# Kernel optimization log

Measured on AMD Instinct MI355X. Metric: run time of the kernel, lower is better.

Reference implementation:

```python
import jax, jax.numpy as jnp
import numpy as np

NEG = -1e9
ALPHA = 0.2  # LeakyReLU slope


def layer_norm(x, scale, bias, eps=1e-5):
    mu = jnp.mean(x, axis=-1, keepdims=True)
    var = jnp.mean(jnp.square(x - mu), axis=-1, keepdims=True)
    return (x - mu) * jax.lax.rsqrt(var + eps) * scale + bias


def gat_layer(x, adj, W, a):
    # x: (b, n, f_in); W: (h, f_in, d_k); a: (h, 2*d_k, 1); adj: (b, n, n) int
    d_k = W.shape[-1]
    h = jnp.einsum('bni,hio->bhno', x, W)            # (b, h, n, d_k)
    a_src = a[:, :d_k, 0]                            # (h, d_k)
    a_dst = a[:, d_k:, 0]                            # (h, d_k)
    # e[b,h,i,j] = leakyrelu(a_src.h_i + a_dst.h_j) -- split form of a.[h_i||h_j]
    src = jnp.einsum('bhnd,hd->bhn', h, a_src)
    dst = jnp.einsum('bhnd,hd->bhn', h, a_dst)
    e = jax.nn.leaky_relu(src[:, :, :, None] + dst[:, :, None, :], ALPHA)
    e = jnp.where(adj[:, None, :, :] == 0, NEG, e)   # mask non-edges
    att = jax.nn.softmax(e, axis=-1)                 # (b, h, n, n)
    return jnp.einsum('bhnm,bhmd->bhnd', att, h)     # (b, h, n, d_k)


def setup_inputs() -> dict:
    key = jax.random.key(0)
    ks = jax.random.split(key, 8)
    B, N, F_IN, HID, OUT, H = 4, 2048, 128, 256, 256, 4
    dk1 = HID // H
    dk2 = OUT // H
    xavier = lambda k, shp: jax.random.uniform(
        k, shp, jnp.float32, -1.0, 1.0) * np.sqrt(6.0 / (shp[-2] + shp[-1]))
    return {
        'node_features': jax.random.normal(ks[0], (B, N, F_IN), jnp.float32),
        'adjacency_matrix': jax.random.randint(ks[1], (B, N, N), 0, 2, jnp.int32),
        'Wp': jax.random.normal(ks[2], (F_IN, HID), jnp.float32) / np.sqrt(F_IN),
        'bp': jnp.zeros((HID,), jnp.float32),
        'W1': xavier(ks[3], (H, HID, dk1)),
        'a1': xavier(ks[4], (H, 2 * dk1, 1)),
        'ln1_s': jnp.ones((HID,), jnp.float32),
        'ln1_b': jnp.zeros((HID,), jnp.float32),
        'W2': xavier(ks[5], (H, HID, dk2)),
        'a2': xavier(ks[6], (H, 2 * dk2, 1)),
        'ln2_s': jnp.ones((dk2,), jnp.float32),
        'ln2_b': jnp.zeros((dk2,), jnp.float32),
    }


def reference(node_features, adjacency_matrix, Wp, bp, W1, a1, ln1_s, ln1_b,
              W2, a2, ln2_s, ln2_b):
    # input projection (dropout is identity in eval mode)
    x = node_features @ Wp + bp                       # (b, n, hid)
    b, n, _ = x.shape

    # layer 1: concat heads, LN, ELU, residual
    hp = gat_layer(x, adjacency_matrix, W1, a1)       # (b, h, n, dk1)
    x1 = hp.reshape(b, n, -1)                         # memory-order reshape (matches torch .view)
    x1 = layer_norm(x1, ln1_s, ln1_b)
    x1 = jax.nn.elu(x1)
    x = x + x1                                        # same shape -> residual

    # layer 2: mean over heads, LN
    hp = gat_layer(x, adjacency_matrix, W2, a2)       # (b, h, n, dk2)
    x2 = hp.mean(axis=1)                              # (b, n, dk2)
    x2 = layer_norm(x2, ln2_s, ln2_b)
    return x2
```

## Files before the change

kernel.cpp:

```cpp
#include <hip/hip_runtime.h>
#include <hip/hip_bf16.h>
#include <hip/hip_fp16.h>

#define BB   4
#define NN   2048
#define FIN  128
#define HD   256
#define NH   4
#define DK   64
#define NEGV (-1000000000.0f)
#define LOG2E 1.4426950408889634f

typedef _Float16 f16x8 __attribute__((ext_vector_type(8)));
typedef _Float16 f16x4 __attribute__((ext_vector_type(4)));
typedef __fp16   h16x2 __attribute__((ext_vector_type(2)));
typedef __fp16   h16x4 __attribute__((ext_vector_type(4)));
typedef __fp16   h16x8 __attribute__((ext_vector_type(8)));
typedef float    f32x16 __attribute__((ext_vector_type(16)));
typedef unsigned long long u64;

__device__ __forceinline__ int SWZ9(int b){ return b ^ (((b >> 9) & 7) << 4); }
__device__ __forceinline__ int SWZ8(int b){ return b ^ (((b >> 8) & 7) << 4); }

__device__ __forceinline__ float fexp2(float x){
#if __has_builtin(__builtin_amdgcn_exp2f)
  return __builtin_amdgcn_exp2f(x);
#else
  return __exp2f(x);
#endif
}

__device__ __forceinline__ f16x8 pack8(float4 a, float4 b){
  f16x8 r;
  r[0]=(_Float16)a.x; r[1]=(_Float16)a.y; r[2]=(_Float16)a.z; r[3]=(_Float16)a.w;
  r[4]=(_Float16)b.x; r[5]=(_Float16)b.y; r[6]=(_Float16)b.z; r[7]=(_Float16)b.w;
  return r;
}

__global__ void __launch_bounds__(256) k_setup(const int* __restrict__ adj,
                                               const float* __restrict__ Wp,
                                               const float* __restrict__ W1,
                                               const float* __restrict__ a1,
                                               const float* __restrict__ W2,
                                               const float* __restrict__ a2,
                                               u64* __restrict__ maskT,
                                               _Float16* __restrict__ WTF,
                                               _Float16* __restrict__ WpF,
                                               float* __restrict__ aS){
  int bid = blockIdx.x;
  int t = threadIdx.x;
  if (bid < 2048){
    int w = t >> 6, lane = t & 63;
    int row = bid*4 + w;
    int b = row >> 11, n = row & (NN-1);
    const int4* ar = (const int4*)(adj + (size_t)row*NN);
    int g = lane >> 4, q = lane & 15;
    #pragma unroll 2
    for (int step = 0; step < 8; ++step){
      int4 v = ar[step*64 + lane];
      unsigned nib = (unsigned)((v.x!=0) | ((v.y!=0)<<1) | ((v.z!=0)<<2) | ((v.w!=0)<<3));
      unsigned lo = (q < 8) ? (nib << (q*4)) : 0u;
      unsigned hi = (q < 8) ? 0u : (nib << ((q-8)*4));
      #pragma unroll
      for (int off = 1; off < 16; off <<= 1){
        lo |= __shfl_xor(lo, off);
        hi |= __shfl_xor(hi, off);
      }
      if (q == 0) maskT[(size_t)(b*32 + step*4 + g)*NN + n] = ((u64)hi << 32) | lo;
    }
  } else if (bid < 2056){
    int qq = bid - 2048;
    int lay = qq >> 2, hh = qq & 3;
    const float* W = (lay ? W2 : W1) + (size_t)hh*HD*DK;
    const float* a = (lay ? a2 : a1) + (size_t)hh*2*DK;
    _Float16* wf = WTF + (size_t)qq*32*512;
    int j = t*2;
    int l5 = j >> 4, lh = (j >> 3) & 1, e = j & 7;
    #pragma unroll 4
    for (int f = 0; f < 32; ++f){
      int kk = f >> 1, dh = f & 1;
      wf[f*512 + j]     = (_Float16)W[(kk*16 + lh*8 + e    )*DK + dh*32 + l5];
      wf[f*512 + j + 1] = (_Float16)W[(kk*16 + lh*8 + e + 1)*DK + dh*32 + l5];
    }
    if (t < 128) aS[(size_t)qq*128 + t] = a[t] * LOG2E;
  } else {
    int kk = bid - 2056;
    int j = t*2;
    int l5 = j >> 4, lh = (j >> 3) & 1, e = j & 7;
    #pragma unroll 4
    for (int cs = 0; cs < 8; ++cs){
      WpF[(kk*8 + cs)*512 + j]     = (_Float16)Wp[(kk*16 + lh*8 + e    )*HD + cs*32 + l5];
      WpF[(kk*8 + cs)*512 + j + 1] = (_Float16)Wp[(kk*16 + lh*8 + e + 1)*HD + cs*32 + l5];
    }
  }
}

template<int L1>
__global__ void __launch_bounds__(256) k_head4(const float* __restrict__ xin,
                                               const _Float16* __restrict__ WpF,
                                               const _Float16* __restrict__ WTF,
                                               const float* __restrict__ aS,
                                               const float* __restrict__ bp,
                                               float* __restrict__ xout,
                                               _Float16* __restrict__ hT,
                                               float* __restrict__ src,
                                               float* __restrict__ dst){
  int nt = blockIdx.x & 31;
  int bh = blockIdx.x >> 5;
  int b = bh >> 2, hh = bh & 3;
  int n0 = nt * 64;
  int t = threadIdx.x;
  int w = t >> 6, l = t & 63, lh = l >> 5, l5 = l & 31;
  int wr = w >> 1, wc = w & 1;

  __shared__ __align__(16) char sm[50176];

  if (L1){
    {
      int r = t >> 2, c0 = (t & 3) * 32;
      const float* np = xin + ((size_t)(b*NN) + n0 + r)*FIN + c0;
      #pragma unroll
      for (int u = 0; u < 4; ++u){
        float4 v0 = *(const float4*)&np[u*8];
        float4 v1 = *(const float4*)&np[u*8 + 4];
        *(f16x8*)&sm[32768 + SWZ8(r*256 + (c0 + u*8)*2)] = pack8(v0, v1);
      }
    }
    __syncthreads();
    f32x16 p00 = {}, p01 = {}, p10 = {}, p11 = {};
    #pragma unroll
    for (int kk = 0; kk < 8; ++kk){
      int ab = (kk*16 + lh*8)*2;
      f16x8 A0 = *(const f16x8*)&sm[32768 + SWZ8(l5*256 + ab)];
      f16x8 A1 = *(const f16x8*)&sm[32768 + SWZ8((32 + l5)*256 + ab)];
      const char* bf = (const char*)WpF + (size_t)(kk*8 + w*2)*1024 + l5*32 + lh*16;
      f16x8 B0 = *(const f16x8*)bf;
      f16x8 B1 = *(const f16x8*)(bf + 1024);
      p00 = __builtin_amdgcn_mfma_f32_32x32x16_f16(A0, B0, p00, 0, 0, 0);
      p01 = __builtin_amdgcn_mfma_f32_32x32x16_f16(A0, B1, p01, 0, 0, 0);
      p10 = __builtin_amdgcn_mfma_f32_32x32x16_f16(A1, B0, p10, 0, 0, 0);
      p11 = __builtin_amdgcn_mfma_f32_32x32x16_f16(A1, B1, p11, 0, 0, 0);
    }
    int c0a = w*64 + l5;
    float bp0 = bp[c0a], bp1 = bp[c0a + 32];
    size_t ro = ((size_t)(b*NN) + n0)*HD;
    #pragma unroll
    for (int g = 0; g < 16; ++g){
      int rr = (g & 3) + 8*(g >> 2) + 4*lh;
      float v00 = p00[g] + bp0, v01 = p01[g] + bp1;
      float v10 = p10[g] + bp0, v11 = p11[g] + bp1;
      *(_Float16*)&sm[SWZ9(rr*512 + c0a*2)]             = (_Float16)v00;
      *(_Float16*)&sm[SWZ9(rr*512 + (c0a + 32)*2)]      = (_Float16)v01;
      *(_Float16*)&sm[SWZ9((rr+32)*512 + c0a*2)]        = (_Float16)v10;
      *(_Float16*)&sm[SWZ9((rr+32)*512 + (c0a + 32)*2)] = (_Float16)v11;
      if (hh == 0){
        xout[ro + (size_t)rr*HD + c0a]           = v00;
        xout[ro + (size_t)rr*HD + c0a + 32]      = v01;
        xout[ro + (size_t)(rr+32)*HD + c0a]      = v10;
        xout[ro + (size_t)(rr+32)*HD + c0a + 32] = v11;
      }
    }
    __syncthreads();
  } else {
    int r = t >> 2, ks = (t & 3) * 64;
    const float* xp = &xin[((size_t)(b*NN) + n0 + r)*HD + ks];
    #pragma unroll
    for (int u = 0; u < 8; ++u){
      float4 v0 = *(const float4*)&xp[u*8];
      float4 v1 = *(const float4*)&xp[u*8 + 4];
      *(f16x8*)&sm[SWZ9(r*512 + (ks + u*8)*2)] = pack8(v0, v1);
    }
    __syncthreads();
  }

  f32x16 hA = {}, hB = {};
  const char* wtb = (const char*)WTF + (size_t)hh*32768 + wc*1024 + l5*32 + lh*16;
  #pragma unroll
  for (int kk = 0; kk < 16; kk += 2){
    int ab0 = (kk*16 + lh*8)*2;
    int ab1 = ((kk+1)*16 + lh*8)*2;
    f16x8 A0 = *(const f16x8*)&sm[SWZ9((wr*32 + l5)*512 + ab0)];
    f16x8 A1 = *(const f16x8*)&sm[SWZ9((wr*32 + l5)*512 + ab1)];
    f16x8 B0 = *(const f16x8*)(wtb + (size_t)kk*2048);
    f16x8 B1 = *(const f16x8*)(wtb + (size_t)(kk+1)*2048);
    hA = __builtin_amdgcn_mfma_f32_32x32x16_f16(A0, B0, hA, 0, 0, 0);
    hB = __builtin_amdgcn_mfma_f32_32x32x16_f16(A1, B1, hB, 0, 0, 0);
  }
  f32x16 acc = hA + hB;

  __syncthreads();
  _Float16* ls = (_Float16*)sm;
  int col = wc*32 + l5;
  float as = aS[(size_t)hh*128 + col];
  float ad = aS[(size_t)hh*128 + 64 + col];
  float* sd = (float*)(sm + 49152);
  #pragma unroll
  for (int g = 0; g < 16; ++g){
    int row = wr*32 + (g & 3) + 8*(g >> 2) + 4*lh;
    ls[col*80 + row] = (_Float16)acc[g];
    float sv = acc[g] * as;
    float dv = acc[g] * ad;
    #pragma unroll
    for (int o = 16; o >= 1; o >>= 1){ sv += __shfl_xor(sv, o); dv += __shfl_xor(dv, o); }
    if (l5 == 0){
      sd[wc*64 + row]       = sv;
      sd[128 + wc*64 + row] = dv;
    }
  }
  __syncthreads();
  int dd = t >> 2, part = t & 3;
  f16x8 o0 = *(const f16x8*)&ls[dd*80 + part*16];
  f16x8 o1 = *(const f16x8*)&ls[dd*80 + part*16 + 8];
  int base = part*1024 + (dd >> 5)*512 + (dd & 31)*16;
  _Float16* op = hT + (size_t)bh*131072 + (size_t)nt*4096 + base;
  *(f16x8*)op = o0;
  *(f16x8*)(op + 8) = o1;
  if (t < 64){
    src[bh*NN + n0 + t] = sd[t] + sd[64 + t];
    dst[bh*NN + n0 + t] = sd[128 + t] + sd[192 + t];
  }
}

__global__ void __launch_bounds__(256, 4) k_attn8(const float* __restrict__ src,
                                                  const float* __restrict__ dst,
                                                  const _Float16* __restrict__ hT,
                                                  const u64* __restrict__ maskT,
                                                  _Float16* __restrict__ accB,
                                                  float* __restrict__ psB){
  int ms = blockIdx.x & 1;
  int rb = (blockIdx.x >> 1) & 63;
  int bh = blockIdx.x >> 7;
  int b  = bh >> 2;
  int n0 = rb * 32;
  int t = threadIdx.x;
  int w = t >> 6, l = t & 63;
  int lh = l >> 5, l5 = l & 31;

  __shared__ __align__(16) char smem[9728];
  __shared__ float rs[4][32];
  __shared__ float red[4];
  float* dstS = (float*)smem;
  float* cs   = (float*)smem;

  {
    const float* dp = dst + bh*NN;
    float4 a = *(const float4*)&dp[t*4];
    float4 bq = *(const float4*)&dp[1024 + t*4];
    float mloc = fmaxf(fmaxf(fmaxf(a.x,a.y), fmaxf(a.z,a.w)),
                       fmaxf(fmaxf(bq.x,bq.y), fmaxf(bq.z,bq.w)));
    *(float4*)&dstS[t*4] = ms ? bq : a;
    #pragma unroll
    for (int o = 32; o >= 1; o >>= 1) mloc = fmaxf(mloc, __shfl_xor(mloc, o));
    if (l == 0) red[w] = mloc;
  }
  __syncthreads();
  float Mbh = fmaxf(fmaxf(red[0], red[1]), fmaxf(red[2], red[3]));
  float srcv = src[bh*NN + n0 + l5];
  float bv = srcv + Mbh;
  float bnd = fmaxf(bv, 0.2f*bv);
  float2 ps2 = make_float2(0.f, 0.f);
  f32x16 acc0 = {}, acc1 = {};

  int kb = w*16 + lh*8;
  const u64* mp = maskT + (size_t)(b*32 + ms*16)*NN + n0 + l5;
  const char* gB0 = (const char*)hT + (size_t)bh*262144 + ms*131072
                    + w*2048 + l5*32 + lh*16;

  u64 mkS0 = mp[0];
  f16x8 B0S0 = *(const f16x8*)(gB0);
  f16x8 B1S0 = *(const f16x8*)(gB0 + 1024);
  u64 mkS1 = mp[NN];
  f16x8 B0S1 = *(const f16x8*)(gB0 + 8192);
  f16x8 B1S1 = *(const f16x8*)(gB0 + 8192 + 1024);
  __builtin_amdgcn_sched_barrier(0);

  #pragma unroll
  for (int mt = 0; mt < 16; ++mt){
    u64 mkC = mkS0;
    f16x8 B0C = B0S0, B1C = B1S0;
    mkS0 = mkS1; B0S0 = B0S1; B1S0 = B1S1;
    if (mt < 14){
      mkS1 = mp[(size_t)(mt+2)*NN];
      B0S1 = *(const f16x8*)(gB0 + (size_t)(mt+2)*8192);
      B1S1 = *(const f16x8*)(gB0 + (size_t)(mt+2)*8192 + 1024);
    }
    __builtin_amdgcn_sched_barrier(0);
    float4 dq0 = *(const float4*)&dstS[mt*64 + kb];
    float4 dq1 = *(const float4*)&dstS[mt*64 + kb + 4];
    unsigned bits = (unsigned)(mkC >> kb) & 0xFFu;
    float dvals[8] = {dq0.x,dq0.y,dq0.z,dq0.w,dq1.x,dq1.y,dq1.z,dq1.w};
    h16x2 hp0, hp1, hp2, hp3;
    {
      float e0 = srcv + dvals[0], e1 = srcv + dvals[1];
      e0 = fmaxf(e0, 0.2f*e0); e1 = fmaxf(e1, 0.2f*e1);
      e0 = (bits & 1u) ? e0 : NEGV;  e1 = (bits & 2u) ? e1 : NEGV;
      float p0 = fexp2(e0 - bnd), p1 = fexp2(e1 - bnd);
      ps2.x += p0; ps2.y += p1;
      hp0 = __builtin_amdgcn_cvt_pkrtz(p0, p1);
    }
    {
      float e0 = srcv + dvals[2], e1 = srcv + dvals[3];
      e0 = fmaxf(e0, 0.2f*e0); e1 = fmaxf(e1, 0.2f*e1);
      e0 = (bits & 4u) ? e0 : NEGV;  e1 = (bits & 8u) ? e1 : NEGV;
      float p0 = fexp2(e0 - bnd), p1 = fexp2(e1 - bnd);
      ps2.x += p0; ps2.y += p1;
      hp1 = __builtin_amdgcn_cvt_pkrtz(p0, p1);
    }
    {
      float e0 = srcv + dvals[4], e1 = srcv + dvals[5];
      e0 = fmaxf(e0, 0.2f*e0); e1 = fmaxf(e1, 0.2f*e1);
      e0 = (bits & 16u) ? e0 : NEGV;  e1 = (bits & 32u) ? e1 : NEGV;
      float p0 = fexp2(e0 - bnd), p1 = fexp2(e1 - bnd);
      ps2.x += p0; ps2.y += p1;
      hp2 = __builtin_amdgcn_cvt_pkrtz(p0, p1);
    }
    {
      float e0 = srcv + dvals[6], e1 = srcv + dvals[7];
      e0 = fmaxf(e0, 0.2f*e0); e1 = fmaxf(e1, 0.2f*e1);
      e0 = (bits & 64u) ? e0 : NEGV;  e1 = (bits & 128u) ? e1 : NEGV;
      float p0 = fexp2(e0 - bnd), p1 = fexp2(e1 - bnd);
      ps2.x += p0; ps2.y += p1;
      hp3 = __builtin_amdgcn_cvt_pkrtz(p0, p1);
    }
    h16x4 lo4 = __builtin_shufflevector(hp0, hp1, 0, 1, 2, 3);
    h16x4 hi4 = __builtin_shufflevector(hp2, hp3, 0, 1, 2, 3);
    h16x8 a8  = __builtin_shufflevector(lo4, hi4, 0, 1, 2, 3, 4, 5, 6, 7);
    f16x8 A   = __builtin_bit_cast(f16x8, a8);
    acc0 = __builtin_amdgcn_mfma_f32_32x32x16_f16(A, B0C, acc0, 0, 0, 0);
    acc1 = __builtin_amdgcn_mfma_f32_32x32x16_f16(A, B1C, acc1, 0, 0, 0);
  }

  float psum = ps2.x + ps2.y;
  psum += __shfl_xor(psum, 32);
  if (l < 32) rs[w][l5] = psum;
  __syncthreads();
  _Float16* accO = accB + (size_t)ms*2097152;
  float* psO  = psB + (size_t)ms*32768;
  if (t < 32) psO[bh*NN + n0 + t] = rs[0][t] + rs[1][t] + rs[2][t] + rs[3][t];
  #pragma unroll 1
  for (int ww = 1; ww < 4; ++ww){
    if (w == ww){
      float* base = cs + l*36;
      *(f32x16*)(base)      = acc0;
      *(f32x16*)(base + 16) = acc1;
    }
    __syncthreads();
    if (w == 0){
      const float* base = cs + l*36;
      acc0 += *(const f32x16*)(base);
      acc1 += *(const f32x16*)(base + 16);
    }
    __syncthreads();
  }
  if (w == 0){
    #pragma unroll
    for (int g = 0; g < 16; ++g){
      int row = (g & 3) + 8*(g >> 2) + 4*lh;
      size_t o = ((size_t)bh*NN + n0 + row)*DK;
      accO[o + l5]      = (_Float16)acc0[g];
      accO[o + 32 + l5] = (_Float16)acc1[g];
    }
  }
}

__global__ void __launch_bounds__(256) k_ln1(const _Float16* __restrict__ a0,
                                             const _Float16* __restrict__ a1,
                                             const float* __restrict__ p0,
                                             const float* __restrict__ p1,
                                             const float* __restrict__ sc,
                                             const float* __restrict__ bi,
                                             float* __restrict__ x){
  int j = blockIdx.x & (NN-1);
  int b = blockIdx.x / NN;
  int c = threadIdx.x;
  int w = c >> 6, l = c & 63;
  int hh = j >> 9;
  int node = ((j & 511) << 2) + w;
  size_t ridx = (size_t)(b*NH + hh)*NN + node;
  float inv = 1.f / (p0[ridx] + p1[ridx]);
  size_t idx = ridx*DK + l;
  float v = ((float)a0[idx] + (float)a1[idx]) * inv;
  __shared__ float red[8];
  float s = v;
  #pragma unroll
  for (int o = 32; o >= 1; o >>= 1) s += __shfl_xor(s, o);
  if (l == 0) red[w] = s;
  __syncthreads();
  float mu = (red[0]+red[1]+red[2]+red[3]) * (1.f/HD);
  float dv = v - mu;
  float q = dv*dv;
  #pragma unroll
  for (int o = 32; o >= 1; o >>= 1) q += __shfl_xor(q, o);
  if (l == 0) red[4+w] = q;
  __syncthreads();
  float var = (red[4]+red[5]+red[6]+red[7]) * (1.f/HD);
  float ln = dv * rsqrtf(var + 1e-5f) * sc[c] + bi[c];
  float el = (ln > 0.f) ? ln : (__expf(ln) - 1.f);
  x[(size_t)blockIdx.x*HD + c] += el;
}

__global__ void __launch_bounds__(256) k_final(const _Float16* __restrict__ a0,
                                               const _Float16* __restrict__ a1,
                                               const float* __restrict__ p0,
                                               const float* __restrict__ p1,
                                               const float* __restrict__ sc,
                                               const float* __restrict__ bi,
                                               float* __restrict__ out){
  int w = threadIdx.x >> 6; int d = threadIdx.x & 63;
  int bn = blockIdx.x*4 + w;
  int b = bn / NN; int n = bn & (NN-1);
  float v = 0.f;
  #pragma unroll
  for (int hh = 0; hh < NH; ++hh){
    size_t ridx = (size_t)(b*NH + hh)*NN + n;
    float inv = 1.f / (p0[ridx] + p1[ridx]);
    size_t idx = ridx*DK + d;
    v += ((float)a0[idx] + (float)a1[idx]) * inv;
  }
  v *= 0.25f;
  float s = v;
  #pragma unroll
  for (int o = 32; o >= 1; o >>= 1) s += __shfl_xor(s, o);
  float mu = s * (1.f/DK);
  float dv = v - mu;
  float q = dv*dv;
  #pragma unroll
  for (int o = 32; o >= 1; o >>= 1) q += __shfl_xor(q, o);
  float var = q * (1.f/DK);
  float ln = dv * rsqrtf(var + 1e-5f) * sc[d] + bi[d];
  out[(size_t)bn*DK + d] = ln;
}

extern "C" void kernel_launch(void* const* d_in, const int* in_sizes, int n_in,
                              void* d_out, int out_size, void* d_ws, size_t ws_size,
                              hipStream_t stream){
  const float* nf   = (const float*)d_in[0];
  const int*   adj  = (const int*)d_in[1];
  const float* Wp   = (const float*)d_in[2];
  const float* bp   = (const float*)d_in[3];
  const float* W1   = (const float*)d_in[4];
  const float* a1   = (const float*)d_in[5];
  const float* ln1s = (const float*)d_in[6];
  const float* ln1b = (const float*)d_in[7];
  const float* W2   = (const float*)d_in[8];
  const float* a2   = (const float*)d_in[9];
  const float* ln2s = (const float*)d_in[10];
  const float* ln2b = (const float*)d_in[11];

  float* ws   = (float*)d_ws;
  float* x    = ws;
  _Float16* accF = (_Float16*)(ws + 2097152);
  float* srcb = ws + 3*2097152;
  float* dstb = srcb + 32768;
  float* psA  = dstb + 32768;
  _Float16* hT = (_Float16*)(psA + 2*32768);
  u64* maskT  = (u64*)(hT + 2097152);
  _Float16* WTF = (_Float16*)(maskT + 262144);
  _Float16* WpF = WTF + 131072;
  float* aS   = (float*)(WpF + 32768);

  _Float16* accH0 = accF;
  _Float16* accH1 = accF + 2097152;
  float* psH0  = psA;
  float* psH1  = psA + 32768;

  k_setup   <<<2064,        256, 0, stream>>>(adj, Wp, W1, a1, W2, a2,
                                              maskT, WTF, WpF, aS);
  k_head4<1><<<BB*NH*NN/64, 256, 0, stream>>>(nf, WpF, WTF,        aS,       bp, x, hT, srcb, dstb);
  k_attn8   <<<BB*NH*NN/16, 256, 0, stream>>>(srcb, dstb, hT, maskT, accF, psA);
  k_ln1     <<<BB*NN,       256, 0, stream>>>(accH0, accH1, psH0, psH1, ln1s, ln1b, x);
  k_head4<0><<<BB*NH*NN/64, 256, 0, stream>>>(x, WpF, WTF + 65536, aS + 512, bp, x, hT, srcb, dstb);
  k_attn8   <<<BB*NH*NN/16, 256, 0, stream>>>(srcb, dstb, hT, maskT, accF, psA);
  k_final   <<<BB*NN/4,     256, 0, stream>>>(accH0, accH1, psH0, psH1, ln2s, ln2b, (float*)d_out);
}
```

Before: 119.1 us.

## Process 64 rows per attention block and spill per-wave partials to global

The attention kernel now handles two 32-row tiles per block, so each loaded B fragment of h feeds four MFMAs instead of two. The in-block cross-wave reduction through shared memory, with its barriers, is removed. Each wave instead writes its own fp16 partial accumulator and row sums into one of eight global slices, and the LN kernels sum those eight slices. The prefetch depth drops from two stages to one, and occupancy is bounded at 3 blocks per SM. In exchange, partial-output traffic to global memory grows roughly fourfold.

```diff
diff --git a/kernel.cpp b/kernel.cpp
--- a/kernel.cpp
+++ b/kernel.cpp
@@ -12,7 +12,6 @@
 #define LOG2E 1.4426950408889634f
 
 typedef _Float16 f16x8 __attribute__((ext_vector_type(8)));
-typedef _Float16 f16x4 __attribute__((ext_vector_type(4)));
 typedef __fp16   h16x2 __attribute__((ext_vector_type(2)));
 typedef __fp16   h16x4 __attribute__((ext_vector_type(4)));
 typedef __fp16   h16x8 __attribute__((ext_vector_type(8)));
@@ -35,6 +34,47 @@
   r[0]=(_Float16)a.x; r[1]=(_Float16)a.y; r[2]=(_Float16)a.z; r[3]=(_Float16)a.w;
   r[4]=(_Float16)b.x; r[5]=(_Float16)b.y; r[6]=(_Float16)b.z; r[7]=(_Float16)b.w;
   return r;
+}
+
+__device__ __forceinline__ f16x8 mkfrag(float srcv, float bnd, unsigned bits,
+                                        float4 dq0, float4 dq1, float2& ps){
+  h16x2 h0, h1, h2, h3;
+  {
+    float e0 = srcv + dq0.x, e1 = srcv + dq0.y;
+    e0 = fmaxf(e0, 0.2f*e0); e1 = fmaxf(e1, 0.2f*e1);
+    e0 = (bits & 1u) ? e0 : NEGV;  e1 = (bits & 2u) ? e1 : NEGV;
+    float p0 = fexp2(e0 - bnd), p1 = fexp2(e1 - bnd);
+    ps.x += p0; ps.y += p1;
+    h0 = __builtin_amdgcn_cvt_pkrtz(p0, p1);
+  }
+  {
+    float e0 = srcv + dq0.z, e1 = srcv + dq0.w;
+    e0 = fmaxf(e0, 0.2f*e0); e1 = fmaxf(e1, 0.2f*e1);
+    e0 = (bits & 4u) ? e0 : NEGV;  e1 = (bits & 8u) ? e1 : NEGV;
+    float p0 = fexp2(e0 - bnd), p1 = fexp2(e1 - bnd);
+    ps.x += p0; ps.y += p1;
+    h1 = __builtin_amdgcn_cvt_pkrtz(p0, p1);
+  }
+  {
+    float e0 = srcv + dq1.x, e1 = srcv + dq1.y;
+    e0 = fmaxf(e0, 0.2f*e0); e1 = fmaxf(e1, 0.2f*e1);
+    e0 = (bits & 16u) ? e0 : NEGV;  e1 = (bits & 32u) ? e1 : NEGV;
+    float p0 = fexp2(e0 - bnd), p1 = fexp2(e1 - bnd);
+    ps.x += p0; ps.y += p1;
+    h2 = __builtin_amdgcn_cvt_pkrtz(p0, p1);
+  }
+  {
+    float e0 = srcv + dq1.z, e1 = srcv + dq1.w;
+    e0 = fmaxf(e0, 0.2f*e0); e1 = fmaxf(e1, 0.2f*e1);
+    e0 = (bits & 64u) ? e0 : NEGV;  e1 = (bits & 128u) ? e1 : NEGV;
+    float p0 = fexp2(e0 - bnd), p1 = fexp2(e1 - bnd);
+    ps.x += p0; ps.y += p1;
+    h3 = __builtin_amdgcn_cvt_pkrtz(p0, p1);
+  }
+  h16x4 lo4 = __builtin_shufflevector(h0, h1, 0, 1, 2, 3);
+  h16x4 hi4 = __builtin_shufflevector(h2, h3, 0, 1, 2, 3);
+  h16x8 a8  = __builtin_shufflevector(lo4, hi4, 0, 1, 2, 3, 4, 5, 6, 7);
+  return __builtin_bit_cast(f16x8, a8);
 }
 
 __global__ void __launch_bounds__(256) k_setup(const int* __restrict__ adj,
@@ -221,26 +261,23 @@
   }
 }
 
-__global__ void __launch_bounds__(256, 4) k_attn8(const float* __restrict__ src,
+__global__ void __launch_bounds__(256, 3) k_attn9(const float* __restrict__ src,
                                                   const float* __restrict__ dst,
                                                   const _Float16* __restrict__ hT,
                                                   const u64* __restrict__ maskT,
-                                                  _Float16* __restrict__ accB,
-                                                  float* __restrict__ psB){
+                                                  _Float16* __restrict__ accG,
+                                                  float* __restrict__ psG){
   int ms = blockIdx.x & 1;
-  int rb = (blockIdx.x >> 1) & 63;
-  int bh = blockIdx.x >> 7;
+  int rb = (blockIdx.x >> 1) & 31;
+  int bh = blockIdx.x >> 6;
   int b  = bh >> 2;
-  int n0 = rb * 32;
+  int n0 = rb * 64;
   int t = threadIdx.x;
   int w = t >> 6, l = t & 63;
   int lh = l >> 5, l5 = l & 31;
 
-  __shared__ __align__(16) char smem[9728];
-  __shared__ float rs[4][32];
+  __shared__ __align__(16) float dstS[1024];
   __shared__ float red[4];
-  float* dstS = (float*)smem;
-  float* cs   = (float*)smem;
 
   {
     const float* dp = dst + bh*NN;
@@ -255,118 +292,71 @@
   }
   __syncthreads();
   float Mbh = fmaxf(fmaxf(red[0], red[1]), fmaxf(red[2], red[3]));
-  float srcv = src[bh*NN + n0 + l5];
-  float bv = srcv + Mbh;
-  float bnd = fmaxf(bv, 0.2f*bv);
-  float2 ps2 = make_float2(0.f, 0.f);
-  f32x16 acc0 = {}, acc1 = {};
+  float srcvA = src[bh*NN + n0 + l5];
+  float srcvB = src[bh*NN + n0 + 32 + l5];
+  float bvA = srcvA + Mbh, bvB = srcvB + Mbh;
+  float bndA = fmaxf(bvA, 0.2f*bvA);
+  float bndB = fmaxf(bvB, 0.2f*bvB);
+  float2 psA2 = make_float2(0.f, 0.f), psB2 = make_float2(0.f, 0.f);
+  f32x16 a0a = {}, a1a = {}, a0b = {}, a1b = {};
 
   int kb = w*16 + lh*8;
-  const u64* mp = maskT + (size_t)(b*32 + ms*16)*NN + n0 + l5;
+  const u64* mpA = maskT + (size_t)(b*32 + ms*16)*NN + n0 + l5;
+  const u64* mpB = mpA + 32;
   const char* gB0 = (const char*)hT + (size_t)bh*262144 + ms*131072
                     + w*2048 + l5*32 + lh*16;
 
-  u64 mkS0 = mp[0];
-  f16x8 B0S0 = *(const f16x8*)(gB0);
-  f16x8 B1S0 = *(const f16x8*)(gB0 + 1024);
-  u64 mkS1 = mp[NN];
-  f16x8 B0S1 = *(const f16x8*)(gB0 + 8192);
-  f16x8 B1S1 = *(const f16x8*)(gB0 + 8192 + 1024);
+  u64 mkAN = mpA[0], mkBN = mpB[0];
+  f16x8 B0N = *(const f16x8*)gB0;
+  f16x8 B1N = *(const f16x8*)(gB0 + 1024);
   __builtin_amdgcn_sched_barrier(0);
 
   #pragma unroll
   for (int mt = 0; mt < 16; ++mt){
-    u64 mkC = mkS0;
-    f16x8 B0C = B0S0, B1C = B1S0;
-    mkS0 = mkS1; B0S0 = B0S1; B1S0 = B1S1;
-    if (mt < 14){
-      mkS1 = mp[(size_t)(mt+2)*NN];
-      B0S1 = *(const f16x8*)(gB0 + (size_t)(mt+2)*8192);
-      B1S1 = *(const f16x8*)(gB0 + (size_t)(mt+2)*8192 + 1024);
+    u64 mkA = mkAN, mkB = mkBN;
+    f16x8 B0 = B0N, B1 = B1N;
+    if (mt < 15){
+      mkAN = mpA[(size_t)(mt+1)*NN];
+      mkBN = mpB[(size_t)(mt+1)*NN];
+      B0N = *(const f16x8*)(gB0 + (size_t)(mt+1)*8192);
+      B1N = *(const f16x8*)(gB0 + (size_t)(mt+1)*8192 + 1024);
     }
     __builtin_amdgcn_sched_barrier(0);
     float4 dq0 = *(const float4*)&dstS[mt*64 + kb];
     float4 dq1 = *(const float4*)&dstS[mt*64 + kb + 4];
-    unsigned bits = (unsigned)(mkC >> kb) & 0xFFu;
-    float dvals[8] = {dq0.x,dq0.y,dq0.z,dq0.w,dq1.x,dq1.y,dq1.z,dq1.w};
-    h16x2 hp0, hp1, hp2, hp3;
-    {
-      float e0 = srcv + dvals[0], e1 = srcv + dvals[1];
-      e0 = fmaxf(e0, 0.2f*e0); e1 = fmaxf(e1, 0.2f*e1);
-      e0 = (bits & 1u) ? e0 : NEGV;  e1 = (bits & 2u) ? e1 : NEGV;
-      float p0 = fexp2(e0 - bnd), p1 = fexp2(e1 - bnd);
-      ps2.x += p0; ps2.y += p1;
-      hp0 = __builtin_amdgcn_cvt_pkrtz(p0, p1);
-    }
-    {
-      float e0 = srcv + dvals[2], e1 = srcv + dvals[3];
-      e0 = fmaxf(e0, 0.2f*e0); e1 = fmaxf(e1, 0.2f*e1);
-      e0 = (bits & 4u) ? e0 : NEGV;  e1 = (bits & 8u) ? e1 : NEGV;
-      float p0 = fexp2(e0 - bnd), p1 = fexp2(e1 - bnd);
-      ps2.x += p0; ps2.y += p1;
-      hp1 = __builtin_amdgcn_cvt_pkrtz(p0, p1);
-    }
-    {
-      float e0 = srcv + dvals[4], e1 = srcv + dvals[5];
-      e0 = fmaxf(e0, 0.2f*e0); e1 = fmaxf(e1, 0.2f*e1);
-      e0 = (bits & 16u) ? e0 : NEGV;  e1 = (bits & 32u) ? e1 : NEGV;
-      float p0 = fexp2(e0 - bnd), p1 = fexp2(e1 - bnd);
-      ps2.x += p0; ps2.y += p1;
-      hp2 = __builtin_amdgcn_cvt_pkrtz(p0, p1);
-    }
-    {
-      float e0 = srcv + dvals[6], e1 = srcv + dvals[7];
-      e0 = fmaxf(e0, 0.2f*e0); e1 = fmaxf(e1, 0.2f*e1);
-      e0 = (bits & 64u) ? e0 : NEGV;  e1 = (bits & 128u) ? e1 : NEGV;
-      float p0 = fexp2(e0 - bnd), p1 = fexp2(e1 - bnd);
-      ps2.x += p0; ps2.y += p1;
-      hp3 = __builtin_amdgcn_cvt_pkrtz(p0, p1);
-    }
-    h16x4 lo4 = __builtin_shufflevector(hp0, hp1, 0, 1, 2, 3);
-    h16x4 hi4 = __builtin_shufflevector(hp2, hp3, 0, 1, 2, 3);
-    h16x8 a8  = __builtin_shufflevector(lo4, hi4, 0, 1, 2, 3, 4, 5, 6, 7);
-    f16x8 A   = __builtin_bit_cast(f16x8, a8);
-    acc0 = __builtin_amdgcn_mfma_f32_32x32x16_f16(A, B0C, acc0, 0, 0, 0);
-    acc1 = __builtin_amdgcn_mfma_f32_32x32x16_f16(A, B1C, acc1, 0, 0, 0);
-  }
-
-  float psum = ps2.x + ps2.y;
-  psum += __shfl_xor(psum, 32);
-  if (l < 32) rs[w][l5] = psum;
-  __syncthreads();
-  _Float16* accO = accB + (size_t)ms*2097152;
-  float* psO  = psB + (size_t)ms*32768;
-  if (t < 32) psO[bh*NN + n0 + t] = rs[0][t] + rs[1][t] + rs[2][t] + rs[3][t];
-  #pragma unroll 1
-  for (int ww = 1; ww < 4; ++ww){
-    if (w == ww){
-      float* base = cs + l*36;
-      *(f32x16*)(base)      = acc0;
-      *(f32x16*)(base + 16) = acc1;
-    }
-    __syncthreads();
-    if (w == 0){
-      const float* base = cs + l*36;
-      acc0 += *(const f32x16*)(base);
-      acc1 += *(const f32x16*)(base + 16);
-    }
-    __syncthreads();
-  }
-  if (w == 0){
-    #pragma unroll
-    for (int g = 0; g < 16; ++g){
-      int row = (g & 3) + 8*(g >> 2) + 4*lh;
-      size_t o = ((size_t)bh*NN + n0 + row)*DK;
-      accO[o + l5]      = (_Float16)acc0[g];
-      accO[o + 32 + l5] = (_Float16)acc1[g];
-    }
-  }
-}
-
-__global__ void __launch_bounds__(256) k_ln1(const _Float16* __restrict__ a0,
-                                             const _Float16* __restrict__ a1,
-                                             const float* __restrict__ p0,
-                                             const float* __restrict__ p1,
+    unsigned bitsA = (unsigned)(mkA >> kb) & 0xFFu;
+    unsigned bitsB = (unsigned)(mkB >> kb) & 0xFFu;
+    f16x8 Aa = mkfrag(srcvA, bndA, bitsA, dq0, dq1, psA2);
+    f16x8 Ab = mkfrag(srcvB, bndB, bitsB, dq0, dq1, psB2);
+    a0a = __builtin_amdgcn_mfma_f32_32x32x16_f16(Aa, B0, a0a, 0, 0, 0);
+    a1a = __builtin_amdgcn_mfma_f32_32x32x16_f16(Aa, B1, a1a, 0, 0, 0);
+    a0b = __builtin_amdgcn_mfma_f32_32x32x16_f16(Ab, B0, a0b, 0, 0, 0);
+    a1b = __builtin_amdgcn_mfma_f32_32x32x16_f16(Ab, B1, a1b, 0, 0, 0);
+  }
+
+  float psA = psA2.x + psA2.y;  psA += __shfl_xor(psA, 32);
+  float psB = psB2.x + psB2.y;  psB += __shfl_xor(psB, 32);
+  int s = w*2 + ms;
+  _Float16* accO = accG + (size_t)s*2097152;
+  float* psO = psG + (size_t)s*32768;
+  if (l < 32){
+    psO[bh*NN + n0 + l5]      = psA;
+    psO[bh*NN + n0 + 32 + l5] = psB;
+  }
+  #pragma unroll
+  for (int g = 0; g < 16; ++g){
+    int row = (g & 3) + 8*(g >> 2) + 4*lh;
+    size_t oA = ((size_t)bh*NN + n0 + row)*DK;
+    size_t oB = ((size_t)bh*NN + n0 + 32 + row)*DK;
+    accO[oA + l5]      = (_Float16)a0a[g];
+    accO[oA + 32 + l5] = (_Float16)a1a[g];
+    accO[oB + l5]      = (_Float16)a0b[g];
+    accO[oB + 32 + l5] = (_Float16)a1b[g];
+  }
+}
+
+__global__ void __launch_bounds__(256) k_ln1(const _Float16* __restrict__ accG,
+                                             const float* __restrict__ psG,
                                              const float* __restrict__ sc,
                                              const float* __restrict__ bi,
                                              float* __restrict__ x){
@@ -377,14 +367,20 @@
   int hh = j >> 9;
   int node = ((j & 511) << 2) + w;
   size_t ridx = (size_t)(b*NH + hh)*NN + node;
-  float inv = 1.f / (p0[ridx] + p1[ridx]);
+  float den = 0.f;
+  #pragma unroll
+  for (int s = 0; s < 8; ++s) den += psG[(size_t)s*32768 + ridx];
+  float inv = 1.f / den;
   size_t idx = ridx*DK + l;
-  float v = ((float)a0[idx] + (float)a1[idx]) * inv;
+  float v = 0.f;
+  #pragma unroll
+  for (int s = 0; s < 8; ++s) v += (float)accG[(size_t)s*2097152 + idx];
+  v *= inv;
   __shared__ float red[8];
-  float s = v;
-  #pragma unroll
-  for (int o = 32; o >= 1; o >>= 1) s += __shfl_xor(s, o);
-  if (l == 0) red[w] = s;
+  float sm_ = v;
+  #pragma unroll
+  for (int o = 32; o >= 1; o >>= 1) sm_ += __shfl_xor(sm_, o);
+  if (l == 0) red[w] = sm_;
   __syncthreads();
   float mu = (red[0]+red[1]+red[2]+red[3]) * (1.f/HD);
   float dv = v - mu;
@@ -399,10 +395,8 @@
   x[(size_t)blockIdx.x*HD + c] += el;
 }
 
-__global__ void __launch_bounds__(256) k_final(const _Float16* __restrict__ a0,
-                                               const _Float16* __restrict__ a1,
-                                               const float* __restrict__ p0,
-                                               const float* __restrict__ p1,
+__global__ void __launch_bounds__(256) k_final(const _Float16* __restrict__ accG,
+                                               const float* __restrict__ psG,
                                                const float* __restrict__ sc,
                                                const float* __restrict__ bi,
                                                float* __restrict__ out){
@@ -413,15 +407,20 @@
   #pragma unroll
   for (int hh = 0; hh < NH; ++hh){
     size_t ridx = (size_t)(b*NH + hh)*NN + n;
-    float inv = 1.f / (p0[ridx] + p1[ridx]);
+    float den = 0.f;
+    #pragma unroll
+    for (int s = 0; s < 8; ++s) den += psG[(size_t)s*32768 + ridx];
     size_t idx = ridx*DK + d;
-    v += ((float)a0[idx] + (float)a1[idx]) * inv;
+    float a = 0.f;
+    #pragma unroll
+    for (int s = 0; s < 8; ++s) a += (float)accG[(size_t)s*2097152 + idx];
+    v += a / den;
   }
   v *= 0.25f;
-  float s = v;
-  #pragma unroll
-  for (int o = 32; o >= 1; o >>= 1) s += __shfl_xor(s, o);
-  float mu = s * (1.f/DK);
+  float sm_ = v;
+  #pragma unroll
+  for (int o = 32; o >= 1; o >>= 1) sm_ += __shfl_xor(sm_, o);
+  float mu = sm_ * (1.f/DK);
   float dv = v - mu;
   float q = dv*dv;
   #pragma unroll
@@ -449,27 +448,22 @@
 
   float* ws   = (float*)d_ws;
   float* x    = ws;
-  _Float16* accF = (_Float16*)(ws + 2097152);
-  float* srcb = ws + 3*2097152;
+  _Float16* accG = (_Float16*)(ws + 2097152);
+  float* srcb = ws + 2097152 + 8388608;
   float* dstb = srcb + 32768;
-  float* psA  = dstb + 32768;
-  _Float16* hT = (_Float16*)(psA + 2*32768);
+  float* psG  = dstb + 32768;
+  _Float16* hT = (_Float16*)(psG + 8*32768);
   u64* maskT  = (u64*)(hT + 2097152);
   _Float16* WTF = (_Float16*)(maskT + 262144);
   _Float16* WpF = WTF + 131072;
   float* aS   = (float*)(WpF + 32768);
 
-  _Float16* accH0 = accF;
-  _Float16* accH1 = accF + 2097152;
-  float* psH0  = psA;
-  float* psH1  = psA + 32768;
-
   k_setup   <<<2064,        256, 0, stream>>>(adj, Wp, W1, a1, W2, a2,
                                               maskT, WTF, WpF, aS);
   k_head4<1><<<BB*NH*NN/64, 256, 0, stream>>>(nf, WpF, WTF,        aS,       bp, x, hT, srcb, dstb);
-  k_attn8   <<<BB*NH*NN/16, 256, 0, stream>>>(srcb, dstb, hT, maskT, accF, psA);
-  k_ln1     <<<BB*NN,       256, 0, stream>>>(accH0, accH1, psH0, psH1, ln1s, ln1b, x);
+  k_attn9   <<<BB*NH*NN/32, 256, 0, stream>>>(srcb, dstb, hT, maskT, accG, psG);
+  k_ln1     <<<BB*NN,       256, 0, stream>>>(accG, psG, ln1s, ln1b, x);
   k_head4<0><<<BB*NH*NN/64, 256, 0, stream>>>(x, WpF, WTF + 65536, aS + 512, bp, x, hT, srcb, dstb);
-  k_attn8   <<<BB*NH*NN/16, 256, 0, stream>>>(srcb, dstb, hT, maskT, accF, psA);
-  k_final   <<<BB*NN/4,     256, 0, stream>>>(accH0, accH1, psH0, psH1, ln2s, ln2b, (float*)d_out);
-}
+  k_attn9   <<<BB*NH*NN/32, 256, 0, stream>>>(srcb, dstb, hT, maskT, accG, psG);
+  k_final   <<<BB*NN/4,     256, 0, stream>>>(accG, psG, ln2s, ln2b, (float*)d_out);
+}
```

New measurement: 124.2 us. +4.3%, slower.
